# Optimization experiments

Measured on AMD Instinct MI355X. Metric: run time of the kernel, lower is better.

## Reference

```python
import jax, jax.numpy as jnp
import numpy as np

B, T, C, HD = 4, 4096, 1024, 64

def setup_inputs() -> dict:
    key = jax.random.key(0)
    k1, k2, k3, k4 = jax.random.split(key, 4)
    x = jax.random.normal(k1, (B, T, C), dtype=jnp.float32)
    scale = 1.0 / np.sqrt(C)
    Wq = jax.random.normal(k2, (C, HD), dtype=jnp.float32) * scale
    Wk = jax.random.normal(k3, (C, HD), dtype=jnp.float32) * scale
    Wv = jax.random.normal(k4, (C, HD), dtype=jnp.float32) * scale
    return {"x": x, "Wq": Wq, "Wk": Wk, "Wv": Wv}

def reference(x, Wq, Wk, Wv):
    # q,k,v: [B,T,HD]
    q = jnp.einsum('btc,ch->bth', x, Wq)
    k = jnp.einsum('btc,ch->bth', x, Wk)
    v = jnp.einsum('btc,ch->bth', x, Wv)
    hd = q.shape[-1]
    scores = jnp.einsum('bth,bsh->bts', q, k) / jnp.sqrt(jnp.float32(hd))  # [B,T,T]
    causal = jnp.tril(jnp.ones((scores.shape[1], scores.shape[1]), dtype=bool))
    scores = jnp.where(causal, scores, -jnp.inf)
    attn = jax.nn.softmax(scores, axis=-1)
    return jnp.einsum('bts,bsh->bth', attn, v)  # [B,T,HD]
```

## Files before the change

kernel.cpp:

```cpp
#include <hip/hip_runtime.h>
#include <hip/hip_bf16.h>

typedef __attribute__((ext_vector_type(8))) short bf16x8;
typedef __attribute__((ext_vector_type(4))) short bf16x4;
typedef __attribute__((ext_vector_type(4))) float f32x4;
typedef __attribute__((ext_vector_type(4))) int   i32x4;

#define C2LOG 0.18033688011112042f
#define THR_RAW 44.3616f

__device__ __forceinline__ short f2bf(float f) {
    union { float f; unsigned u; } v; v.f = f;
    unsigned r = v.u + 0x7fff + ((v.u >> 16) & 1);
    return (short)(r >> 16);
}
__device__ __forceinline__ unsigned cvtpk(float lo, float hi) {
    unsigned r;
    asm("v_cvt_pk_bf16_f32 %0, %1, %2" : "=v"(r) : "v"(lo), "v"(hi));
    return r;
}
__device__ __forceinline__ float bf2f(short s) {
    union { unsigned u; float f; } v; v.u = ((unsigned)(unsigned short)s) << 16;
    return v.f;
}

#define BB 4
#define TT 4096
#define CC 1024
#define HD 64
#define NTASK_PB 144
#define NTASK (BB * NTASK_PB)

__global__ void prep_w(const float* __restrict__ Wq, const float* __restrict__ Wk,
                       const float* __restrict__ Wv, short* __restrict__ Wt) {
    const int n = blockIdx.x;
    const float* W = (n < 64) ? Wq : (n < 128) ? Wk : Wv;
    const int col = n & 63;
    for (int k = threadIdx.x; k < CC; k += blockDim.x)
        Wt[n * CC + k] = f2bf(W[k * HD + col]);
}

__global__ __launch_bounds__(512) void proj_qkv(const float* __restrict__ x,
        const short* __restrict__ Wt, short* __restrict__ Q,
        short* __restrict__ K, short* __restrict__ Vt) {
    __shared__ short xs[2][32 * 72];
    __shared__ short wsm[2][192 * 64];

    const int tid  = threadIdx.x;
    const int lane = tid & 63;
    const int wv   = tid >> 6;
    const int lm   = lane & 15;
    const int lg   = lane >> 4;
    const int mhalf = wv & 1;
    const int ngrp  = wv >> 1;
    const int mbase = blockIdx.x * 32;

    const int xr  = tid >> 4;
    const int xq4 = tid & 15;
    const float* xrow = x + (size_t)(mbase + xr) * CC;

    int wsrow[3], wscol[3];
    #pragma unroll
    for (int it = 0; it < 3; ++it) {
        const int off = it * 8192 + wv * 1024 + lane * 16;
        wsrow[it] = off >> 7;
        wscol[it] = (off & 127) ^ ((wsrow[it] & 7) << 4);
    }

#define STAGE_W(bufidx, kc)                                                           \
    {                                                                                 \
        _Pragma("unroll")                                                             \
        for (int it = 0; it < 3; ++it) {                                              \
            const char* src = (const char*)(Wt + (size_t)wsrow[it] * CC + (kc) * 64)  \
                              + wscol[it];                                            \
            char* dst = (char*)&wsm[bufidx][0] + it * 8192 + wv * 1024;               \
            __builtin_amdgcn_global_load_lds(                                         \
                (const __attribute__((address_space(1))) unsigned*)src,               \
                (__attribute__((address_space(3))) unsigned*)dst, 16, 0, 0);          \
        }                                                                             \
    }

#define CONV_X(bufidx, xv)                                                            \
    {                                                                                 \
        int2 pk;                                                                      \
        pk.x = (int)cvtpk((xv).x, (xv).y);                                            \
        pk.y = (int)cvtpk((xv).z, (xv).w);                                            \
        *reinterpret_cast<int2*>(&xs[bufidx][xr * 72 + xq4 * 4]) = pk;                \
    }

    f32x4 acc[3];
    #pragma unroll
    for (int i = 0; i < 3; ++i) acc[i] = f32x4{0.f, 0.f, 0.f, 0.f};

    {
        float4 v = *reinterpret_cast<const float4*>(xrow + xq4 * 4);
        CONV_X(0, v)
        STAGE_W(0, 0)
    }
    asm volatile("s_waitcnt vmcnt(0)" ::: "memory");
    __syncthreads();

    const int arow = mhalf * 16 + lm;
    int buf = 0;
    for (int kc = 0; kc < 16; ++kc) {
        float4 nv;
        const bool more = (kc < 15);
        if (more) {
            nv = *reinterpret_cast<const float4*>(xrow + (kc + 1) * 64 + xq4 * 4);
            STAGE_W(buf ^ 1, kc + 1)
        }

        bf16x8 a0 = *reinterpret_cast<const bf16x8*>(&xs[buf][arow * 72 + lg * 8]);
        bf16x8 a1 = *reinterpret_cast<const bf16x8*>(&xs[buf][arow * 72 + 32 + lg * 8]);
        #pragma unroll
        for (int c = 0; c < 3; ++c) {
            const int brow = (ngrp * 3 + c) * 16 + lm;
            const int sw = (brow & 7) << 4;
            bf16x8 b0 = *reinterpret_cast<const bf16x8*>(
                (const char*)&wsm[buf][0] + brow * 128 + ((lg * 16) ^ sw));
            bf16x8 b1 = *reinterpret_cast<const bf16x8*>(
                (const char*)&wsm[buf][0] + brow * 128 + ((64 + lg * 16) ^ sw));
            acc[c] = __builtin_amdgcn_mfma_f32_16x16x32_bf16(a0, b0, acc[c], 0, 0, 0);
            acc[c] = __builtin_amdgcn_mfma_f32_16x16x32_bf16(a1, b1, acc[c], 0, 0, 0);
        }

        if (more) CONV_X(buf ^ 1, nv)
        asm volatile("s_waitcnt vmcnt(0)" ::: "memory");
        __syncthreads();
        buf ^= 1;
    }
#undef STAGE_W
#undef CONV_X

    const int mrow = mbase + mhalf * 16 + lg * 4;
    #pragma unroll
    for (int c = 0; c < 3; ++c) {
        const int cn = ngrp * 3 + c;
        if (cn < 4) {
            #pragma unroll
            for (int r = 0; r < 4; ++r)
                Q[(size_t)(mrow + r) * HD + cn * 16 + lm] = f2bf(acc[c][r]);
        } else if (cn < 8) {
            #pragma unroll
            for (int r = 0; r < 4; ++r)
                K[(size_t)(mrow + r) * HD + (cn - 4) * 16 + lm] = f2bf(acc[c][r]);
        } else {
            const int bb   = mbase >> 12;
            const int tloc = (mbase & 4095) + mhalf * 16 + lg * 4;
            int2 pk;
            pk.x = (int)cvtpk(acc[c][0], acc[c][1]);
            pk.y = (int)cvtpk(acc[c][2], acc[c][3]);
            *reinterpret_cast<int2*>(
                Vt + (size_t)bb * (HD * TT) + (size_t)((cn - 8) * 16 + lm) * TT + tloc) = pk;
        }
    }
}

__global__ __launch_bounds__(256, 3) void attn(const short* __restrict__ Q,
        const short* __restrict__ K, const short* __restrict__ Vt,
        short* __restrict__ Opart, float* __restrict__ Mpart,
        float* __restrict__ Lpart) {
    __shared__ short ks[2][64 * 64];
    __shared__ short vs[2][64 * 64];

    const int tid  = threadIdx.x;
    const int lane = tid & 63;
    const int wv   = tid >> 6;
    const int lm   = lane & 15;
    const int lg   = lane >> 4;

    const int task = blockIdx.x;
    const int b  = task / NTASK_PB;
    int t_in = task - b * NTASK_PB;
    int g = 0;
    while (t_in >= 2 * (g + 1) * (g + 2)) ++g;
    const int idx = t_in - 2 * g * (g + 1);
    const int i   = 4 * g + idx / (g + 1);
    const int seg = idx % (g + 1);
    const int S   = g + 1;
    const int niter = 2 * i + 2;

    const size_t qkb = (size_t)b * TT * HD;
    const size_t vtb = (size_t)b * HD * TT;
    const int qrow = i * 128 + wv * 32;
    const int tmax = (qrow + 31) >> 6;

    bf16x8 qf0 = *reinterpret_cast<const bf16x8*>(Q + qkb + (size_t)(qrow + lm) * HD + lg * 8);
    bf16x8 qf1 = *reinterpret_cast<const bf16x8*>(Q + qkb + (size_t)(qrow + lm) * HD + 32 + lg * 8);
    bf16x8 qf2 = *reinterpret_cast<const bf16x8*>(Q + qkb + (size_t)(qrow + 16 + lm) * HD + lg * 8);
    bf16x8 qf3 = *reinterpret_cast<const bf16x8*>(Q + qkb + (size_t)(qrow + 16 + lm) * HD + 32 + lg * 8);

    f32x4 oA[4], oB[4];
    #pragma unroll
    for (int c = 0; c < 4; ++c) { oA[c] = f32x4{0.f,0.f,0.f,0.f}; oB[c] = f32x4{0.f,0.f,0.f,0.f}; }
    float mrunA = -1e30f, lrunA = 0.f;
    float mrunB = -1e30f, lrunB = 0.f;

    const int srcA = lm + ((lane & 16) << 1);
    const int srcB = srcA + 16;
    const bool hihalf = (lane & 32) != 0;

    int srow[2], scol[2];
    #pragma unroll
    for (int c = 0; c < 2; ++c) {
        const int off = wv * 2048 + c * 1024 + lane * 16;
        srow[c] = off >> 7;
        scol[c] = (off & 127) ^ ((srow[c] & 7) << 4);
    }

#define STAGE_KV(bufidx, tt)                                                          \
    {                                                                                 \
        _Pragma("unroll")                                                             \
        for (int c = 0; c < 2; ++c) {                                                 \
            const char* ksrc = (const char*)(K + qkb) + (tt) * 8192                   \
                               + (srow[c] << 7) + scol[c];                            \
            char* kdst = (char*)&ks[bufidx][0] + wv * 2048 + c * 1024;                \
            __builtin_amdgcn_global_load_lds(                                         \
                (const __attribute__((address_space(1))) unsigned*)ksrc,              \
                (__attribute__((address_space(3))) unsigned*)kdst, 16, 0, 0);         \
            const char* vsrc = (const char*)(Vt + vtb) + (size_t)srow[c] * (TT * 2)   \
                               + (tt) * 128 + scol[c];                                \
            char* vdst = (char*)&vs[bufidx][0] + wv * 2048 + c * 1024;                \
            __builtin_amdgcn_global_load_lds(                                         \
                (const __attribute__((address_space(1))) unsigned*)vsrc,              \
                (__attribute__((address_space(3))) unsigned*)vdst, 16, 0, 0);         \
        }                                                                             \
    }

    STAGE_KV(0, seg)
    asm volatile("s_waitcnt vmcnt(0)" ::: "memory");
    __syncthreads();

    int buf = 0;
    for (int t = seg; t < niter; t += S) {
        const int tn = t + S;
        if (tn < niter) STAGE_KV(buf ^ 1, tn)

        if (t <= tmax) {
            const short* ksb = &ks[buf][0];
            const short* vsb = &vs[buf][0];
            const int kv = t * 64;

            f32x4 stA[4], stB[4];
            #pragma unroll
            for (int kt = 0; kt < 4; ++kt) {
                const int krow = kt * 16 + lm;
                const int sw = (krow & 7) << 4;
                bf16x8 k0 = *reinterpret_cast<const bf16x8*>(
                    (const char*)ksb + krow * 128 + ((lg * 16) ^ sw));
                bf16x8 k1 = *reinterpret_cast<const bf16x8*>(
                    (const char*)ksb + krow * 128 + ((64 + lg * 16) ^ sw));
                f32x4 a = f32x4{0.f,0.f,0.f,0.f};
                a = __builtin_amdgcn_mfma_f32_16x16x32_bf16(k0, qf0, a, 0, 0, 0);
                a = __builtin_amdgcn_mfma_f32_16x16x32_bf16(k1, qf1, a, 0, 0, 0);
                stA[kt] = a;
                f32x4 bb2 = f32x4{0.f,0.f,0.f,0.f};
                bb2 = __builtin_amdgcn_mfma_f32_16x16x32_bf16(k0, qf2, bb2, 0, 0, 0);
                bb2 = __builtin_amdgcn_mfma_f32_16x16x32_bf16(k1, qf3, bb2, 0, 0, 0);
                stB[kt] = bb2;
            }

            if (kv + 63 > qrow) {
                const int qgA = qrow + lm;
                const int qgB = qrow + 16 + lm;
                #pragma unroll
                for (int kt = 0; kt < 4; ++kt)
                    #pragma unroll
                    for (int r = 0; r < 4; ++r) {
                        const int kk = kv + kt * 16 + lg * 4 + r;
                        if (kk > qgA) stA[kt][r] = -1e30f;
                        if (kk > qgB) stB[kt][r] = -1e30f;
                    }
            }

            float mA0 = fmaxf(fmaxf(stA[0][0], stA[0][1]), fmaxf(stA[0][2], stA[0][3]));
            float mA1 = fmaxf(fmaxf(stA[1][0], stA[1][1]), fmaxf(stA[1][2], stA[1][3]));
            float mA2 = fmaxf(fmaxf(stA[2][0], stA[2][1]), fmaxf(stA[2][2], stA[2][3]));
            float mA3 = fmaxf(fmaxf(stA[3][0], stA[3][1]), fmaxf(stA[3][2], stA[3][3]));
            float mlocA = fmaxf(fmaxf(mA0, mA1), fmaxf(mA2, mA3));
            float mB0 = fmaxf(fmaxf(stB[0][0], stB[0][1]), fmaxf(stB[0][2], stB[0][3]));
            float mB1 = fmaxf(fmaxf(stB[1][0], stB[1][1]), fmaxf(stB[1][2], stB[1][3]));
            float mB2 = fmaxf(fmaxf(stB[2][0], stB[2][1]), fmaxf(stB[2][2], stB[2][3]));
            float mB3 = fmaxf(fmaxf(stB[3][0], stB[3][1]), fmaxf(stB[3][2], stB[3][3]));
            float mlocB = fmaxf(fmaxf(mB0, mB1), fmaxf(mB2, mB3));
            mlocA = fmaxf(mlocA, __shfl_xor(mlocA, 16));
            mlocA = fmaxf(mlocA, __shfl_xor(mlocA, 32));
            mlocB = fmaxf(mlocB, __shfl_xor(mlocB, 16));
            mlocB = fmaxf(mlocB, __shfl_xor(mlocB, 32));

            if (!__all(mlocA <= mrunA + THR_RAW)) {
                const float mnewA = fmaxf(mrunA, mlocA);
                const float alphaA = __builtin_amdgcn_exp2f((mrunA - mnewA) * C2LOG);
                mrunA = mnewA;
                lrunA *= alphaA;
                #pragma unroll
                for (int c = 0; c < 4; ++c)
                    #pragma unroll
                    for (int r = 0; r < 4; ++r) oA[c][r] *= alphaA;
            }
            if (!__all(mlocB <= mrunB + THR_RAW)) {
                const float mnewB = fmaxf(mrunB, mlocB);
                const float alphaB = __builtin_amdgcn_exp2f((mrunB - mnewB) * C2LOG);
                mrunB = mnewB;
                lrunB *= alphaB;
                #pragma unroll
                for (int c = 0; c < 4; ++c)
                    #pragma unroll
                    for (int r = 0; r < 4; ++r) oB[c][r] *= alphaB;
            }

            const float ncA = -mrunA * C2LOG;
            const float ncB = -mrunB * C2LOG;
            float pA[4][4], pB[4][4];
            float rsA = 0.f, rsB = 0.f;
            #pragma unroll
            for (int kt = 0; kt < 4; ++kt)
                #pragma unroll
                for (int r = 0; r < 4; ++r) {
                    pA[kt][r] = __builtin_amdgcn_exp2f(__builtin_fmaf(stA[kt][r], C2LOG, ncA));
                    rsA += pA[kt][r];
                    pB[kt][r] = __builtin_amdgcn_exp2f(__builtin_fmaf(stB[kt][r], C2LOG, ncB));
                    rsB += pB[kt][r];
                }
            rsA += __shfl_xor(rsA, 16); rsA += __shfl_xor(rsA, 32);
            rsB += __shfl_xor(rsB, 16); rsB += __shfl_xor(rsB, 32);
            lrunA += rsA;
            lrunB += rsB;

            unsigned uA[4][2], uB[4][2];
            #pragma unroll
            for (int kt = 0; kt < 4; ++kt) {
                uA[kt][0] = cvtpk(pA[kt][0], pA[kt][1]);
                uA[kt][1] = cvtpk(pA[kt][2], pA[kt][3]);
                uB[kt][0] = cvtpk(pB[kt][0], pB[kt][1]);
                uB[kt][1] = cvtpk(pB[kt][2], pB[kt][3]);
            }

            #pragma unroll
            for (int h = 0; h < 2; ++h) {
                const int a0 = __shfl((int)uA[2*h][0],   srcA);
                const int a1c = __shfl((int)uA[2*h+1][0], srcA);
                const int a2 = __shfl((int)uA[2*h][1],   srcA);
                const int a3c = __shfl((int)uA[2*h+1][1], srcA);
                const int a4 = __shfl((int)uA[2*h][0],   srcB);
                const int a5c = __shfl((int)uA[2*h+1][0], srcB);
                const int a6 = __shfl((int)uA[2*h][1],   srcB);
                const int a7c = __shfl((int)uA[2*h+1][1], srcB);
                union { i32x4 iv; bf16x8 v; } cvA;
                cvA.iv = i32x4{ hihalf ? a1c : a0, hihalf ? a3c : a2,
                                hihalf ? a5c : a4, hihalf ? a7c : a6 };
                const int b0 = __shfl((int)uB[2*h][0],   srcA);
                const int b1c = __shfl((int)uB[2*h+1][0], srcA);
                const int b2 = __shfl((int)uB[2*h][1],   srcA);
                const int b3c = __shfl((int)uB[2*h+1][1], srcA);
                const int b4 = __shfl((int)uB[2*h][0],   srcB);
                const int b5c = __shfl((int)uB[2*h+1][0], srcB);
                const int b6 = __shfl((int)uB[2*h][1],   srcB);
                const int b7c = __shfl((int)uB[2*h+1][1], srcB);
                union { i32x4 iv; bf16x8 v; } cvB;
                cvB.iv = i32x4{ hihalf ? b1c : b0, hihalf ? b3c : b2,
                                hihalf ? b5c : b4, hihalf ? b7c : b6 };
                #pragma unroll
                for (int c = 0; c < 4; ++c) {
                    const int vrow = c * 16 + lm;
                    const int sw = (vrow & 7) << 4;
                    bf16x8 va = *reinterpret_cast<const bf16x8*>(
                        (const char*)vsb + vrow * 128 + ((h * 64 + lg * 16) ^ sw));
                    oA[c] = __builtin_amdgcn_mfma_f32_16x16x32_bf16(va, cvA.v, oA[c], 0, 0, 0);
                    oB[c] = __builtin_amdgcn_mfma_f32_16x16x32_bf16(va, cvB.v, oB[c], 0, 0, 0);
                }
            }
        }

        asm volatile("s_waitcnt vmcnt(0)" ::: "memory");
        __syncthreads();
        buf ^= 1;
    }
#undef STAGE_KV

    short* Ob = Opart + (size_t)task * (128 * HD);
    #pragma unroll
    for (int c = 0; c < 4; ++c) {
        int2 pkA, pkB;
        pkA.x = (int)cvtpk(oA[c][0], oA[c][1]);
        pkA.y = (int)cvtpk(oA[c][2], oA[c][3]);
        pkB.x = (int)cvtpk(oB[c][0], oB[c][1]);
        pkB.y = (int)cvtpk(oB[c][2], oB[c][3]);
        *reinterpret_cast<int2*>(&Ob[(wv * 32 + lm) * HD + c * 16 + lg * 4]) = pkA;
        *reinterpret_cast<int2*>(&Ob[(wv * 32 + 16 + lm) * HD + c * 16 + lg * 4]) = pkB;
    }
    if (lg == 0) {
        Mpart[task * 128 + wv * 32 + lm] = mrunA;
        Lpart[task * 128 + wv * 32 + lm] = lrunA;
        Mpart[task * 128 + wv * 32 + 16 + lm] = mrunB;
        Lpart[task * 128 + wv * 32 + 16 + lm] = lrunB;
    }
}

__global__ __launch_bounds__(256) void combine(const short* __restrict__ Opart,
        const float* __restrict__ Mpart, const float* __restrict__ Lpart,
        float* __restrict__ out) {
    const int b   = blockIdx.x >> 8;
    const int rem = blockIdx.x & 255;
    const int i   = rem >> 3;
    const int rr  = rem & 7;
    const int g = i >> 2;
    const int S = g + 1;
    const int task0 = b * NTASK_PB + 2 * g * (g + 1) + (i - 4 * g) * (g + 1);
    const int qbase = i * 128;

    const int tid = threadIdx.x;
    const int row = rr * 16 + (tid >> 4);
    const int cb  = (tid & 15) << 2;

    float mmax = -1e30f;
    float ms[8];
    for (int s = 0; s < S; ++s) {
        ms[s] = Mpart[(task0 + s) * 128 + row];
        mmax = fmaxf(mmax, ms[s]);
    }
    float lsum = 0.f;
    float a0 = 0.f, a1 = 0.f, a2 = 0.f, a3 = 0.f;
    for (int s = 0; s < S; ++s) {
        const float w = __builtin_amdgcn_exp2f((ms[s] - mmax) * C2LOG);
        lsum += Lpart[(task0 + s) * 128 + row] * w;
        bf16x4 ov = *reinterpret_cast<const bf16x4*>(
            &Opart[((size_t)(task0 + s) * 128 + row) * HD + cb]);
        a0 += bf2f(ov[0]) * w;
        a1 += bf2f(ov[1]) * w;
        a2 += bf2f(ov[2]) * w;
        a3 += bf2f(ov[3]) * w;
    }
    const float inv = 1.0f / lsum;
    f32x4 res{ a0 * inv, a1 * inv, a2 * inv, a3 * inv };
    *reinterpret_cast<f32x4*>(
        &out[((size_t)b * TT + qbase + row) * HD + cb]) = res;
}

extern "C" void kernel_launch(void* const* d_in, const int* in_sizes, int n_in,
                              void* d_out, int out_size, void* d_ws, size_t ws_size,
                              hipStream_t stream) {
    const float* x  = (const float*)d_in[0];
    const float* Wq = (const float*)d_in[1];
    const float* Wk = (const float*)d_in[2];
    const float* Wv = (const float*)d_in[3];
    float* out = (float*)d_out;

    char* ws = (char*)d_ws;
    short* Wt    = (short*)(ws);
    short* Q     = (short*)(ws + 393216);
    short* K     = (short*)(ws + 2490368);
    short* Vt    = (short*)(ws + 4587520);
    short* Opart = (short*)(ws + 6684672);
    float* Mpart = (float*)(ws + 16121856);
    float* Lpart = (float*)(ws + 16416768);

    hipLaunchKernelGGL(prep_w,   dim3(192),   dim3(256), 0, stream, Wq, Wk, Wv, Wt);
    hipLaunchKernelGGL(proj_qkv, dim3(512),   dim3(512), 0, stream, x, Wt, Q, K, Vt);
    hipLaunchKernelGGL(attn,     dim3(NTASK), dim3(256), 0, stream, Q, K, Vt,
                       Opart, Mpart, Lpart);
    hipLaunchKernelGGL(combine,  dim3(1024),  dim3(256), 0, stream,
                       Opart, Mpart, Lpart, out);
}
```

Baseline: 65.87 us.

## Load x directly into MFMA A-fragments and tile weight transpose through LDS

The weight prep kernel now transposes W in 64x64 tiles through shared memory with coalesced float4 reads and 16-byte bf16 writes, replacing strided scalar column reads, and launches 48 blocks instead of 192. The projection kernel drops the x shared-memory staging: each lane loads its own A-fragment floats from global memory, converts to bf16 in registers and feeds MFMA directly. This removes LDS writes/reads and bank traffic for x, but each of the 4 row-groups of waves reloads the same x rows and the per-lane global loads are less coalesced. A launch-bounds occupancy hint of 6 is also added.

```diff
diff --git a/kernel.cpp b/kernel.cpp
--- a/kernel.cpp
+++ b/kernel.cpp
@@ -31,19 +31,43 @@
 #define NTASK_PB 144
 #define NTASK (BB * NTASK_PB)
 
-__global__ void prep_w(const float* __restrict__ Wq, const float* __restrict__ Wk,
-                       const float* __restrict__ Wv, short* __restrict__ Wt) {
-    const int n = blockIdx.x;
-    const float* W = (n < 64) ? Wq : (n < 128) ? Wk : Wv;
-    const int col = n & 63;
-    for (int k = threadIdx.x; k < CC; k += blockDim.x)
-        Wt[n * CC + k] = f2bf(W[k * HD + col]);
-}
-
-__global__ __launch_bounds__(512) void proj_qkv(const float* __restrict__ x,
+__global__ __launch_bounds__(256) void prep_w(const float* __restrict__ Wq,
+        const float* __restrict__ Wk, const float* __restrict__ Wv,
+        short* __restrict__ Wt) {
+    __shared__ float wls[64][65];
+    const int w = blockIdx.x >> 4;
+    const int c = blockIdx.x & 15;
+    const float* W = (w == 0) ? Wq : (w == 1) ? Wk : Wv;
+
+    const int r  = threadIdx.x >> 4;
+    const int q4 = threadIdx.x & 15;
+    #pragma unroll
+    for (int rr = 0; rr < 4; ++rr) {
+        const int row = rr * 16 + r;
+        float4 v = *reinterpret_cast<const float4*>(
+            W + (size_t)(c * 64 + row) * HD + q4 * 4);
+        wls[row][q4 * 4 + 0] = v.x;
+        wls[row][q4 * 4 + 1] = v.y;
+        wls[row][q4 * 4 + 2] = v.z;
+        wls[row][q4 * 4 + 3] = v.w;
+    }
+    __syncthreads();
+
+    const int n  = threadIdx.x >> 2;
+    const int ks = (threadIdx.x & 3) * 16;
+    bf16x8 o0, o1;
+    #pragma unroll
+    for (int j = 0; j < 8; ++j) o0[j] = f2bf(wls[ks + j][n]);
+    #pragma unroll
+    for (int j = 0; j < 8; ++j) o1[j] = f2bf(wls[ks + 8 + j][n]);
+    short* dst = Wt + (size_t)(w * 64 + n) * CC + c * 64 + ks;
+    *reinterpret_cast<bf16x8*>(dst)     = o0;
+    *reinterpret_cast<bf16x8*>(dst + 8) = o1;
+}
+
+__global__ __launch_bounds__(512, 6) void proj_qkv(const float* __restrict__ x,
         const short* __restrict__ Wt, short* __restrict__ Q,
         short* __restrict__ K, short* __restrict__ Vt) {
-    __shared__ short xs[2][32 * 72];
     __shared__ short wsm[2][192 * 64];
 
     const int tid  = threadIdx.x;
@@ -55,9 +79,7 @@
     const int ngrp  = wv >> 1;
     const int mbase = blockIdx.x * 32;
 
-    const int xr  = tid >> 4;
-    const int xq4 = tid & 15;
-    const float* xrow = x + (size_t)(mbase + xr) * CC;
+    const float* xr2 = x + (size_t)(mbase + mhalf * 16 + lm) * CC;
 
     int wsrow[3], wscol[3];
     #pragma unroll
@@ -80,38 +102,37 @@
         }                                                                             \
     }
 
-#define CONV_X(bufidx, xv)                                                            \
-    {                                                                                 \
-        int2 pk;                                                                      \
-        pk.x = (int)cvtpk((xv).x, (xv).y);                                            \
-        pk.y = (int)cvtpk((xv).z, (xv).w);                                            \
-        *reinterpret_cast<int2*>(&xs[bufidx][xr * 72 + xq4 * 4]) = pk;                \
-    }
-
     f32x4 acc[3];
     #pragma unroll
     for (int i = 0; i < 3; ++i) acc[i] = f32x4{0.f, 0.f, 0.f, 0.f};
 
-    {
-        float4 v = *reinterpret_cast<const float4*>(xrow + xq4 * 4);
-        CONV_X(0, v)
-        STAGE_W(0, 0)
-    }
+    float4 v0 = *reinterpret_cast<const float4*>(xr2 + lg * 8);
+    float4 v1 = *reinterpret_cast<const float4*>(xr2 + lg * 8 + 4);
+    float4 v2 = *reinterpret_cast<const float4*>(xr2 + 32 + lg * 8);
+    float4 v3 = *reinterpret_cast<const float4*>(xr2 + 32 + lg * 8 + 4);
+    STAGE_W(0, 0)
     asm volatile("s_waitcnt vmcnt(0)" ::: "memory");
     __syncthreads();
 
-    const int arow = mhalf * 16 + lm;
     int buf = 0;
     for (int kc = 0; kc < 16; ++kc) {
-        float4 nv;
+        float4 n0, n1, n2, n3;
         const bool more = (kc < 15);
         if (more) {
-            nv = *reinterpret_cast<const float4*>(xrow + (kc + 1) * 64 + xq4 * 4);
+            const float* xn = xr2 + (kc + 1) * 64;
+            n0 = *reinterpret_cast<const float4*>(xn + lg * 8);
+            n1 = *reinterpret_cast<const float4*>(xn + lg * 8 + 4);
+            n2 = *reinterpret_cast<const float4*>(xn + 32 + lg * 8);
+            n3 = *reinterpret_cast<const float4*>(xn + 32 + lg * 8 + 4);
             STAGE_W(buf ^ 1, kc + 1)
         }
 
-        bf16x8 a0 = *reinterpret_cast<const bf16x8*>(&xs[buf][arow * 72 + lg * 8]);
-        bf16x8 a1 = *reinterpret_cast<const bf16x8*>(&xs[buf][arow * 72 + 32 + lg * 8]);
+        union { i32x4 iv; bf16x8 v; } a0, a1;
+        a0.iv = i32x4{ (int)cvtpk(v0.x, v0.y), (int)cvtpk(v0.z, v0.w),
+                       (int)cvtpk(v1.x, v1.y), (int)cvtpk(v1.z, v1.w) };
+        a1.iv = i32x4{ (int)cvtpk(v2.x, v2.y), (int)cvtpk(v2.z, v2.w),
+                       (int)cvtpk(v3.x, v3.y), (int)cvtpk(v3.z, v3.w) };
+
         #pragma unroll
         for (int c = 0; c < 3; ++c) {
             const int brow = (ngrp * 3 + c) * 16 + lm;
@@ -120,17 +141,16 @@
                 (const char*)&wsm[buf][0] + brow * 128 + ((lg * 16) ^ sw));
             bf16x8 b1 = *reinterpret_cast<const bf16x8*>(
                 (const char*)&wsm[buf][0] + brow * 128 + ((64 + lg * 16) ^ sw));
-            acc[c] = __builtin_amdgcn_mfma_f32_16x16x32_bf16(a0, b0, acc[c], 0, 0, 0);
-            acc[c] = __builtin_amdgcn_mfma_f32_16x16x32_bf16(a1, b1, acc[c], 0, 0, 0);
+            acc[c] = __builtin_amdgcn_mfma_f32_16x16x32_bf16(a0.v, b0, acc[c], 0, 0, 0);
+            acc[c] = __builtin_amdgcn_mfma_f32_16x16x32_bf16(a1.v, b1, acc[c], 0, 0, 0);
         }
 
-        if (more) CONV_X(buf ^ 1, nv)
+        if (more) { v0 = n0; v1 = n1; v2 = n2; v3 = n3; }
         asm volatile("s_waitcnt vmcnt(0)" ::: "memory");
         __syncthreads();
         buf ^= 1;
     }
 #undef STAGE_W
-#undef CONV_X
 
     const int mrow = mbase + mhalf * 16 + lg * 4;
     #pragma unroll
@@ -455,7 +475,7 @@
     float* Mpart = (float*)(ws + 16121856);
     float* Lpart = (float*)(ws + 16416768);
 
-    hipLaunchKernelGGL(prep_w,   dim3(192),   dim3(256), 0, stream, Wq, Wk, Wv, Wt);
+    hipLaunchKernelGGL(prep_w,   dim3(48),    dim3(256), 0, stream, Wq, Wk, Wv, Wt);
     hipLaunchKernelGGL(proj_qkv, dim3(512),   dim3(512), 0, stream, x, Wt, Q, K, Vt);
     hipLaunchKernelGGL(attn,     dim3(NTASK), dim3(256), 0, stream, Q, K, Vt,
                        Opart, Mpart, Lpart);
```

Result: slower. 85.46 us (+29.7%).

## Triple-buffer K/V staging in attention and tile the weight transpose via LDS

Applied to the files above, without the earlier changes.

The attention kernel moves from double to triple-buffered K/V LDS tiles. Loads are issued two iterations ahead, and each iteration waits only on the older loads using partial vmcnt waits and raw s_barrier, so global loads overlap more compute. prep_w now transposes the weights through a 64x65 LDS tile with coalesced float4 reads and 16-byte bf16 writes, instead of strided scalar reads. The extra buffer raises LDS use per block from 32KB to 48KB, which may limit occupancy under the 3-blocks-per-CU launch bound.

```diff
diff --git a/kernel.cpp b/kernel.cpp
--- a/kernel.cpp
+++ b/kernel.cpp
@@ -31,13 +31,38 @@
 #define NTASK_PB 144
 #define NTASK (BB * NTASK_PB)
 
-__global__ void prep_w(const float* __restrict__ Wq, const float* __restrict__ Wk,
-                       const float* __restrict__ Wv, short* __restrict__ Wt) {
-    const int n = blockIdx.x;
-    const float* W = (n < 64) ? Wq : (n < 128) ? Wk : Wv;
-    const int col = n & 63;
-    for (int k = threadIdx.x; k < CC; k += blockDim.x)
-        Wt[n * CC + k] = f2bf(W[k * HD + col]);
+__global__ __launch_bounds__(256) void prep_w(const float* __restrict__ Wq,
+        const float* __restrict__ Wk, const float* __restrict__ Wv,
+        short* __restrict__ Wt) {
+    __shared__ float wls[64][65];
+    const int w = blockIdx.x >> 4;
+    const int c = blockIdx.x & 15;
+    const float* W = (w == 0) ? Wq : (w == 1) ? Wk : Wv;
+
+    const int r  = threadIdx.x >> 4;
+    const int q4 = threadIdx.x & 15;
+    #pragma unroll
+    for (int rr = 0; rr < 4; ++rr) {
+        const int row = rr * 16 + r;
+        float4 v = *reinterpret_cast<const float4*>(
+            W + (size_t)(c * 64 + row) * HD + q4 * 4);
+        wls[row][q4 * 4 + 0] = v.x;
+        wls[row][q4 * 4 + 1] = v.y;
+        wls[row][q4 * 4 + 2] = v.z;
+        wls[row][q4 * 4 + 3] = v.w;
+    }
+    __syncthreads();
+
+    const int n  = threadIdx.x >> 2;
+    const int ks = (threadIdx.x & 3) * 16;
+    bf16x8 o0, o1;
+    #pragma unroll
+    for (int j = 0; j < 8; ++j) o0[j] = f2bf(wls[ks + j][n]);
+    #pragma unroll
+    for (int j = 0; j < 8; ++j) o1[j] = f2bf(wls[ks + 8 + j][n]);
+    short* dst = Wt + (size_t)(w * 64 + n) * CC + c * 64 + ks;
+    *reinterpret_cast<bf16x8*>(dst)     = o0;
+    *reinterpret_cast<bf16x8*>(dst + 8) = o1;
 }
 
 __global__ __launch_bounds__(512) void proj_qkv(const float* __restrict__ x,
@@ -160,8 +185,8 @@
         const short* __restrict__ K, const short* __restrict__ Vt,
         short* __restrict__ Opart, float* __restrict__ Mpart,
         float* __restrict__ Lpart) {
-    __shared__ short ks[2][64 * 64];
-    __shared__ short vs[2][64 * 64];
+    __shared__ short ks[3][64 * 64];
+    __shared__ short vs[3][64 * 64];
 
     const int tid  = threadIdx.x;
     const int lane = tid & 63;
@@ -179,6 +204,7 @@
     const int seg = idx % (g + 1);
     const int S   = g + 1;
     const int niter = 2 * i + 2;
+    const int nloop = (niter - seg + S - 1) / S;
 
     const size_t qkb = (size_t)b * TT * HD;
     const size_t vtb = (size_t)b * HD * TT;
@@ -228,17 +254,22 @@
     }
 
     STAGE_KV(0, seg)
-    asm volatile("s_waitcnt vmcnt(0)" ::: "memory");
-    __syncthreads();
-
-    int buf = 0;
-    for (int t = seg; t < niter; t += S) {
-        const int tn = t + S;
-        if (tn < niter) STAGE_KV(buf ^ 1, tn)
+    if (nloop > 1) {
+        STAGE_KV(1, seg + S)
+        asm volatile("s_waitcnt vmcnt(4)" ::: "memory");
+    } else {
+        asm volatile("s_waitcnt vmcnt(0)" ::: "memory");
+    }
+    __builtin_amdgcn_s_barrier();
+
+    for (int n = 0; n < nloop; ++n) {
+        const int t = seg + n * S;
+        const bool stage2 = (n + 2 < nloop);
+        if (stage2) STAGE_KV((n + 2) % 3, t + 2 * S)
 
         if (t <= tmax) {
-            const short* ksb = &ks[buf][0];
-            const short* vsb = &vs[buf][0];
+            const short* ksb = &ks[n % 3][0];
+            const short* vsb = &vs[n % 3][0];
             const int kv = t * 64;
 
             f32x4 stA[4], stB[4];
@@ -372,9 +403,11 @@
             }
         }
 
-        asm volatile("s_waitcnt vmcnt(0)" ::: "memory");
-        __syncthreads();
-        buf ^= 1;
+        __builtin_amdgcn_sched_barrier(0);
+        asm volatile("s_waitcnt lgkmcnt(0)" ::: "memory");
+        if (stage2) asm volatile("s_waitcnt vmcnt(4)" ::: "memory");
+        else        asm volatile("s_waitcnt vmcnt(0)" ::: "memory");
+        __builtin_amdgcn_s_barrier();
     }
 #undef STAGE_KV
 
@@ -455,7 +488,7 @@
     float* Mpart = (float*)(ws + 16121856);
     float* Lpart = (float*)(ws + 16416768);
 
-    hipLaunchKernelGGL(prep_w,   dim3(192),   dim3(256), 0, stream, Wq, Wk, Wv, Wt);
+    hipLaunchKernelGGL(prep_w,   dim3(48),    dim3(256), 0, stream, Wq, Wk, Wv, Wt);
     hipLaunchKernelGGL(proj_qkv, dim3(512),   dim3(512), 0, stream, x, Wt, Q, K, Vt);
     hipLaunchKernelGGL(attn,     dim3(NTASK), dim3(256), 0, stream, Q, K, Vt,
                        Opart, Mpart, Lpart);
```

After: 66.74 us. No clear change (+1.3%).
